# Optimization experiments

Measured on AMD Instinct MI355X. Metric: run time of the kernel, lower is better.

Reference implementation:

```python
import jax, jax.numpy as jnp
import numpy as np

T, B = 4096, 512


def setup_inputs() -> dict:
    key = jax.random.key(0)
    k = jax.random.split(key, 8)
    f32 = jnp.float32
    labels = jax.random.normal(k[0], (T, B, 1), dtype=f32) * 2.0
    logits = jax.random.uniform(k[1], (T, B, 12), dtype=f32)  # normalized params in [0,1]
    uMotor1 = 300.0 + 200.0 * jax.random.uniform(k[2], (T, B, 1), dtype=f32)
    uMotor2 = 300.0 + 200.0 * jax.random.uniform(k[3], (T, B, 1), dtype=f32)
    uMotor3 = 300.0 + 200.0 * jax.random.uniform(k[4], (T, B, 1), dtype=f32)
    uMotor4 = 300.0 + 200.0 * jax.random.uniform(k[5], (T, B, 1), dtype=f32)
    minMotor = 50.0 + 25.0 * jax.random.uniform(k[6], (T, B, 1), dtype=f32)
    maxMotor = 900.0 + 50.0 * jax.random.uniform(k[7], (T, B, 1), dtype=f32)
    return dict(labels=labels, logits=logits, uMotor1=uMotor1, uMotor2=uMotor2,
                uMotor3=uMotor3, uMotor4=uMotor4, maxMotor=maxMotor, minMotor=minMotor)


def _simulate_loss(labels, logits, uMotor1, uMotor2, uMotor3, uMotor4, maxMotor, minMotor):
    mB, g, tau, IRzz, uP = 1.2, 9.81, 0.005, 1e-4, 1.0
    maxChange, max_inc, eps = 95.0, 400.0, 1e-12
    Tn, Bn, _ = logits.shape
    dt = logits.dtype

    gp = lambda kk: logits[:, :, kk]                      # [T, B]
    scale = lambda kk, base: (1.0 + (0.5 - gp(kk)) * maxChange / 100.0) * base
    dxm = scale(0, 0.16); dym = scale(1, 0.16)
    IBxx = scale(3, 0.0123); IByy = scale(4, 0.0123); IBzz = scale(5, 0.0123)
    Cd = scale(6, 0.1)
    kTh = scale(7, 1.076e-5); kTo = scale(8, 1.632e-7)
    tau2 = scale(9, 0.015); kp = scale(10, 1.0); damp = scale(11, 1.0)

    actual_z = labels[:, :, 0]
    u1 = uMotor1[:, :, 0]; u2 = uMotor2[:, :, 0]
    u3 = uMotor3[:, :, 0]; u4 = uMotor4[:, :, 0]
    mn = minMotor[:, :, 0]; mx = maxMotor[:, :, 0]

    hover = jnp.sqrt(jnp.clip(mB * g / (4.0 * kTh.mean() + eps), 1e-6))
    z = jnp.zeros((Bn,), dt)
    one = jnp.ones((Bn,), dt)
    hv = hover * one
    carry0 = (z, z, z,            # x, y, z position
              one, z, z, z,       # quaternion
              z, z, z,            # xdot, ydot, zdot
              z, z, z,            # p, q, r
              hv, hv, hv, hv,     # motor speeds
              z, z, z, z)         # motor accelerations

    xs = (u1[1:], u2[1:], u3[1:], u4[1:], mn[1:], mx[1:],
          damp[1:], tau2[1:], kp[1:], kTh[1:], kTo[1:], Cd[1:],
          IBxx[1:], IByy[1:], IBzz[1:], dxm[1:], dym[1:])

    def step(carry, x):
        (xx, xy, xz, q0, q1, q2, q3, xd, yd, zd, pv, qv, rv,
         w1, w2, w3, w4, wd1, wd2, wd3, wd4) = carry
        (u1c, u2c, u3c, u4c, mnc, mxc, dampc, tau2c, kpc, kThc, kToc, Cdc,
         IBxxc, IByyc, IBzzc, dxmc, dymc) = x
        # 2nd-order motor dynamics (uses un-clamped speeds)
        wdd1 = -2.0 * dampc * tau2c * wd1 - w1 + kpc * u1c / tau2c ** 2
        wdd2 = -2.0 * dampc * tau2c * wd2 - w2 + kpc * u2c / tau2c ** 2
        wdd3 = -2.0 * dampc * tau2c * wd3 - w3 + kpc * u3c / tau2c ** 2
        wdd4 = -2.0 * dampc * tau2c * wd4 - w4 + kpc * u4c / tau2c ** 2
        w1c = jnp.clip(w1, mnc, mxc); w2c = jnp.clip(w2, mnc, mxc)
        w3c = jnp.clip(w3, mnc, mxc); w4c = jnp.clip(w4, mnc, mxc)
        T1 = kThc * w1c ** 2; T2 = kThc * w2c ** 2
        T3 = kThc * w3c ** 2; T4 = kThc * w4c ** 2
        Q1 = kToc * w1c ** 2; Q2 = kToc * w2c ** 2
        Q3 = kToc * w3c ** 2; Q4 = kToc * w4c ** 2
        Thr = T1 + T2 + T3 + T4
        nxd = xd + tau * (Cdc * jnp.sign(-xd) * xd ** 2 + 2.0 * (q0 * q2 + q1 * q3) * Thr) / mB
        nyd = yd + tau * (Cdc * jnp.sign(-yd) * yd ** 2 - 2.0 * (q0 * q1 - q2 * q3) * Thr) / mB
        nzd = zd + tau * (-Cdc * jnp.sign(zd) * zd ** 2 + Thr * (q0 ** 2 - q1 ** 2 - q2 ** 2 + q3 ** 2) - g * mB) / mB
        nq0 = q0 + tau * (-0.5 * pv * q1 - 0.5 * qv * q2 - 0.5 * rv * q3)
        nq1 = q1 + tau * (0.5 * pv * q0 - 0.5 * qv * q3 + 0.5 * rv * q2)
        nq2 = q2 + tau * (0.5 * pv * q3 + 0.5 * qv * q0 - 0.5 * rv * q1)
        nq3 = q3 + tau * (-0.5 * pv * q2 + 0.5 * qv * q1 + 0.5 * rv * q0)
        wsum = w1c - w2c + w3c - w4c
        npv = pv + tau * ((IByyc - IBzzc) * qv * rv - uP * IRzz * wsum * qv + (T1 - T2 - T3 + T4) * dymc) / IBxxc
        nqv = qv + tau * ((IBzzc - IBxxc) * pv * rv + uP * IRzz * wsum * pv + (T1 + T2 - T3 - T4) * dxmc) / IByyc
        nrv = rv + tau * ((IBxxc - IByyc) * pv * qv - Q1 + Q2 - Q3 + Q4) / IBzzc
        nxx = xx + tau * nxd
        nxy = xy + tau * nyd
        nxz_raw = xz + tau * nzd
        nw1 = w1c + tau * wd1; nw2 = w2c + tau * wd2
        nw3 = w3c + tau * wd3; nw4 = w4c + tau * wd4
        nwd1 = wd1 + tau * wdd1; nwd2 = wd2 + tau * wdd2
        nwd3 = wd3 + tau * wdd3; nwd4 = wd4 + tau * wdd4
        mask = jnp.isfinite(nxz_raw) & (jnp.abs(nxz_raw - xz) <= max_inc)
        nxz = jnp.where(mask, nxz_raw, xz)
        new_carry = (nxx, nxy, nxz, nq0, nq1, nq2, nq3, nxd, nyd, nzd,
                     npv, nqv, nrv, nw1, nw2, nw3, nw4, nwd1, nwd2, nwd3, nwd4)
        return new_carry, nxz

    _, z_traj = jax.lax.scan(step, carry0, xs)           # [T-1, B]
    pred_z = jnp.concatenate([jnp.zeros((1, Bn), dt), z_traj], axis=0)  # [T, B]
    return jnp.mean((pred_z - actual_z) ** 2)


def reference(labels, logits, uMotor1, uMotor2, uMotor3, uMotor4, maxMotor, minMotor):
    return _simulate_loss(labels, logits, uMotor1, uMotor2, uMotor3, uMotor4, maxMotor, minMotor)
```

## Files before the change

### kernel.cpp

```cpp
#include <hip/hip_runtime.h>
#include <math.h>

#define T_STEPS 4096
#define B_N     512
#define CHUNK   6
#define NCHF    682

typedef float f2 __attribute__((ext_vector_type(2)));

__device__ __forceinline__ f2 pk_fma(f2 a, f2 b, f2 c){ f2 d; asm("v_pk_fma_f32 %0, %1, %2, %3" : "=v"(d) : "v"(a), "v"(b), "v"(c)); return d; }
__device__ __forceinline__ f2 pk_mul(f2 a, f2 b){ f2 d; asm("v_pk_mul_f32 %0, %1, %2" : "=v"(d) : "v"(a), "v"(b)); return d; }
__device__ __forceinline__ f2 pk_add(f2 a, f2 b){ f2 d; asm("v_pk_add_f32 %0, %1, %2" : "=v"(d) : "v"(a), "v"(b)); return d; }
__device__ __forceinline__ f2 pk_sub(f2 a, f2 b){ f2 d; asm("v_pk_add_f32 %0, %1, %2 neg_lo:[0,1] neg_hi:[0,1]" : "=v"(d) : "v"(a), "v"(b)); return d; }
__device__ __forceinline__ f2 pk_dd(f2 dP){ f2 d; asm("v_pk_add_f32 %0, %1, %1 op_sel:[0,1] op_sel_hi:[0,1] neg_lo:[0,1] neg_hi:[0,0]" : "=v"(d) : "v"(dP)); return d; }
__device__ __forceinline__ f2 pk_vq(f2 a, f2 b){ f2 d; asm("v_pk_add_f32 %0, %1, %2 op_sel:[0,1] op_sel_hi:[1,0]" : "=v"(d) : "v"(a), "v"(b)); return d; }
__device__ __forceinline__ f2 pk_t01a(f2 pq, f2 qA){ f2 d; asm("v_pk_mul_f32 %0, %1, %2 op_sel:[0,1] op_sel_hi:[0,0]" : "=v"(d) : "v"(pq), "v"(qA)); return d; }
__device__ __forceinline__ f2 pk_t01b(f2 pq, f2 qB, f2 acc){ asm("v_pk_fma_f32 %0, %1, %2, %0 op_sel:[1,0,0] op_sel_hi:[1,1,1] neg_hi:[0,1,0]" : "+v"(acc) : "v"(pq), "v"(qB)); return acc; }
__device__ __forceinline__ f2 pk_t01c(f2 rz, f2 qB, f2 acc){ asm("v_pk_fma_f32 %0, %1, %2, %0 op_sel:[0,1,0] op_sel_hi:[0,0,1]" : "+v"(acc) : "v"(rz), "v"(qB)); return acc; }
__device__ __forceinline__ f2 pk_t23a(f2 pq, f2 qA){ f2 d; asm("v_pk_mul_f32 %0, %1, %2 op_sel:[1,0] op_sel_hi:[1,1]" : "=v"(d) : "v"(pq), "v"(qA)); return d; }
__device__ __forceinline__ f2 pk_t23b(f2 pq, f2 qB, f2 acc){ asm("v_pk_fma_f32 %0, %1, %2, %0 op_sel:[0,1,0] op_sel_hi:[0,0,1] neg_hi:[0,1,0]" : "+v"(acc) : "v"(pq), "v"(qB)); return acc; }
__device__ __forceinline__ f2 pk_t23c(f2 rz, f2 qA, f2 acc){ asm("v_pk_fma_f32 %0, %1, %2, %0 op_sel:[0,1,0] op_sel_hi:[0,0,1] neg_lo:[0,1,0]" : "+v"(acc) : "v"(rz), "v"(qA)); return acc; }
__device__ __forceinline__ f2 pk_s1p(f2 pq, f2 rz){ f2 d; asm("v_pk_mul_f32 %0, %1, %2 op_sel:[1,0] op_sel_hi:[0,0]" : "=v"(d) : "v"(pq), "v"(rz)); return d; }
__device__ __forceinline__ f2 pk_s2p(f2 pq, f2 ws){ f2 d; asm("v_pk_mul_f32 %0, %1, %2 op_sel:[1,0] op_sel_hi:[0,1]" : "=v"(d) : "v"(pq), "v"(ws)); return d; }

union PkU { float4 v[5]; };

struct CarryP {
  f2 w12, w34, wd12, wd34, qA, qB, pq, rz;
  float xz;
};

__device__ __forceinline__ void stepP(CarryP& c, const float4* F, float& facc,
                                      f2 TT, f2 HT, f2 HP) {
  const float TAU = 0.005f, TAUG = 0.04905f;
  f2 KU12 = {F[0].x, F[0].y}, KU34 = {F[0].z, F[0].w};
  f2 AA   = {F[1].x, F[1].y};
  float mn = F[1].z, mx = F[1].w;
  f2 cAC = {F[2].x, F[2].y}, cBD = {F[2].z, F[2].w};
  f2 cdymxm = {F[3].x, F[3].y};
  float cE = F[3].z, cq = F[3].w;
  float cthr = F[4].x, mcdx = F[4].y, label = F[4].z;

  f2 wdd12 = pk_sub(pk_fma(AA, c.wd12, KU12), c.w12);
  f2 wdd34 = pk_sub(pk_fma(AA, c.wd34, KU34), c.w34);
  f2 wc12, wc34;
  wc12.x = fminf(fmaxf(c.w12.x, mn), mx); wc12.y = fminf(fmaxf(c.w12.y, mn), mx);
  wc34.x = fminf(fmaxf(c.w34.x, mn), mx); wc34.y = fminf(fmaxf(c.w34.y, mn), mx);
  f2 s12 = pk_mul(wc12, wc12), s34 = pk_mul(wc34, wc34);
  f2 aP = pk_add(s12, s34);
  f2 dP = pk_sub(s12, s34);
  float ssum = aP.x + aP.y;
  float dqd  = aP.y - aP.x;
  f2 dd = pk_dd(dP);
  f2 tw = pk_add(wc12, wc34);
  float wsum = tw.x - tw.y;
  f2 qs1 = pk_mul(c.qA, c.qA), qs2 = pk_mul(c.qB, c.qB);
  f2 vq = pk_vq(qs1, qs2);
  float qq = vq.x - vq.y;
  float zd = c.rz.y;
  float zdm = zd * fabsf(zd);
  float nzd = fmaf(mcdx, zdm, zd);
  float Thr2 = cthr * ssum;
  nzd = fmaf(Thr2, qq, nzd) - TAUG;
  f2 t01 = pk_t01a(c.pq, c.qA);
  t01 = pk_t01b(c.pq, c.qB, t01);
  t01 = pk_t01c(c.rz, c.qB, t01);
  f2 t23 = pk_t23a(c.pq, c.qA);
  t23 = pk_t23b(c.pq, c.qB, t23);
  t23 = pk_t23c(c.rz, c.qA, t23);
  f2 nqA = pk_fma(HT, t01, c.qA);
  f2 nqB = pk_fma(HP, t23, c.qB);
  f2 sp1 = pk_s1p(c.pq, c.rz);
  f2 ws2 = {wsum, wsum};
  f2 sp2 = pk_s2p(c.pq, ws2);
  f2 npq = pk_fma(cAC, sp1, c.pq);
  npq = pk_fma(cBD, sp2, npq);
  npq = pk_fma(cdymxm, dd, npq);
  float nrv = fmaf(cE, c.pq.x * c.pq.y, c.rz.x);
  nrv = fmaf(cq, dqd, nrv);
  float nxz = fmaf(TAU, nzd, c.xz);
  float dlt = nxz - c.xz;
  float xznew = (fabsf(dlt) <= 400.0f) ? nxz : c.xz;
  float e = xznew - label;
  facc = fmaf(e, e, facc);
  f2 nw12 = pk_fma(TT, c.wd12, wc12);
  f2 nw34 = pk_fma(TT, c.wd34, wc34);
  c.wd12 = pk_fma(TT, wdd12, c.wd12);
  c.wd34 = pk_fma(TT, wdd34, c.wd34);
  c.w12 = nw12; c.w34 = nw34;
  c.qA = nqA; c.qB = nqB; c.pq = npq;
  c.rz = f2{nrv, nzd}; c.xz = xznew;
}

struct Pk {
  float KU1, KU2, KU3, KU4, A, mn, mx, cthr;
  float cdym, cdxm, cq, cdx, cA, cB, cC, cD, cE, label, pad0, pad1;
};
__device__ __forceinline__ float sc_ref(float g, float base) {
  return (1.0f + (0.5f - g) * 0.95f) * base;
}
struct Carry {
  float xz, q0, q1, q2, q3, zd, pv, qv, rv;
  float w1, w2, w3, w4, wd1, wd2, wd3, wd4;
};
__device__ __forceinline__ Pk computePk(size_t i,
    const float* __restrict__ logits,
    const float* __restrict__ u1, const float* __restrict__ u2,
    const float* __restrict__ u3, const float* __restrict__ u4,
    const float* __restrict__ mxM, const float* __restrict__ mnM,
    const float* __restrict__ labels) {
  const float4* lg = (const float4*)logits + i * 3;
  float4 l0 = lg[0], l1 = lg[1], l2 = lg[2];
  float dxm  = sc_ref(l0.x, 0.16f);
  float dym  = sc_ref(l0.y, 0.16f);
  float IBxx = sc_ref(l0.w, 0.0123f);
  float IByy = sc_ref(l1.x, 0.0123f);
  float IBzz = sc_ref(l1.y, 0.0123f);
  float Cd   = sc_ref(l1.z, 0.1f);
  float kTh  = sc_ref(l1.w, 1.076e-05f);
  float kTo  = sc_ref(l2.x, 1.632e-07f);
  float tau2 = sc_ref(l2.y, 0.015f);
  float kp   = sc_ref(l2.z, 1.0f);
  float damp = sc_ref(l2.w, 1.0f);
  const float tau = 0.005f, tauOverMb = tau / 1.2f;
  Pk p;
  float K = kp / (tau2 * tau2);
  p.KU1 = K * u1[i];  p.KU2 = K * u2[i];  p.KU3 = K * u3[i];  p.KU4 = K * u4[i];
  p.A = -2.0f * damp * tau2;
  p.mn = mnM[i];  p.mx = mxM[i];
  p.cthr = kTh * tauOverMb;
  float tx = tau / IBxx, ty = tau / IByy, tz = tau / IBzz;
  p.cdym = kTh * dym * tx;  p.cdxm = kTh * dxm * ty;
  p.cq = kTo * tz;  p.cdx = Cd * tauOverMb;
  p.cA = (IByy - IBzz) * tx;  p.cB = 1e-04f * tx;
  p.cC = (IBzz - IBxx) * ty;  p.cD = 1e-04f * ty;
  p.cE = (IBxx - IByy) * tz;
  p.label = labels[i];  p.pad0 = 0.f; p.pad1 = 0.f;
  return p;
}
__device__ __forceinline__ void stepOne(Carry& c, const Pk& p, float& facc) {
  const float TAU = 0.005f, HTAU = 0.0025f, TAUG = 0.04905f;
  float wdd1 = fmaf(p.A, c.wd1, p.KU1) - c.w1;
  float wdd2 = fmaf(p.A, c.wd2, p.KU2) - c.w2;
  float wdd3 = fmaf(p.A, c.wd3, p.KU3) - c.w3;
  float wdd4 = fmaf(p.A, c.wd4, p.KU4) - c.w4;
  float w1c = fminf(fmaxf(c.w1, p.mn), p.mx);
  float w2c = fminf(fmaxf(c.w2, p.mn), p.mx);
  float w3c = fminf(fmaxf(c.w3, p.mn), p.mx);
  float w4c = fminf(fmaxf(c.w4, p.mn), p.mx);
  float s1 = w1c*w1c, s2 = w2c*w2c, s3 = w3c*w3c, s4 = w4c*w4c;
  float sA = s1+s3, sB = s2+s4, ssum = sA+sB;
  float dymd = (s1+s4)-(s2+s3), dxmd = (s1+s2)-(s3+s4), dqd = sB-sA;
  float Thr2 = p.cthr * ssum;
  float qq = fmaf(c.q0,c.q0,c.q3*c.q3) - fmaf(c.q1,c.q1,c.q2*c.q2);
  float zdm = c.zd * fabsf(c.zd);
  float nzd = fmaf(-p.cdx, zdm, c.zd);
  nzd = fmaf(Thr2, qq, nzd) - TAUG;
  float t0 = fmaf(c.pv,c.q1, fmaf(c.qv,c.q2,  c.rv*c.q3));
  float t1 = fmaf(c.pv,c.q0, fmaf(-c.qv,c.q3, c.rv*c.q2));
  float t2 = fmaf(c.pv,c.q3, fmaf(c.qv,c.q0, -(c.rv*c.q1)));
  float t3 = fmaf(-c.pv,c.q2, fmaf(c.qv,c.q1, c.rv*c.q0));
  float nq0 = fmaf(-HTAU,t0,c.q0), nq1 = fmaf(HTAU,t1,c.q1);
  float nq2 = fmaf(HTAU,t2,c.q2),  nq3 = fmaf(HTAU,t3,c.q3);
  float wsum = (w1c-w2c)+(w3c-w4c);
  float npv = fmaf(p.cA, c.qv*c.rv, c.pv);
  npv = fmaf(-p.cB, wsum*c.qv, npv); npv = fmaf(p.cdym, dymd, npv);
  float nqv = fmaf(p.cC, c.pv*c.rv, c.qv);
  nqv = fmaf(p.cD, wsum*c.pv, nqv);  nqv = fmaf(p.cdxm, dxmd, nqv);
  float nrv = fmaf(p.cE, c.pv*c.qv, c.rv);
  nrv = fmaf(p.cq, dqd, nrv);
  float nxz = fmaf(TAU, nzd, c.xz);
  float d = nxz - c.xz;
  float xznew = (fabsf(d) <= 400.0f) ? nxz : c.xz;
  float e = xznew - p.label;
  facc = fmaf(e, e, facc);
  c.w1 = fmaf(TAU,c.wd1,w1c); c.w2 = fmaf(TAU,c.wd2,w2c);
  c.w3 = fmaf(TAU,c.wd3,w3c); c.w4 = fmaf(TAU,c.wd4,w4c);
  c.wd1 = fmaf(TAU,wdd1,c.wd1); c.wd2 = fmaf(TAU,wdd2,c.wd2);
  c.wd3 = fmaf(TAU,wdd3,c.wd3); c.wd4 = fmaf(TAU,wdd4,c.wd4);
  c.q0=nq0; c.q1=nq1; c.q2=nq2; c.q3=nq3;
  c.pv=npv; c.qv=nqv; c.rv=nrv; c.zd=nzd; c.xz=xznew;
}

__device__ __forceinline__ void gload_lds16(const void* g, void* l) {
  __builtin_amdgcn_global_load_lds(
      (const __attribute__((address_space(1))) void*)g,
      (__attribute__((address_space(3))) void*)l, 16, 0, 0);
}

__global__ void k_kth(const float* __restrict__ logits, float* __restrict__ partial) {
  __shared__ float sm[256];
  float a = 0.f;
  const int n = T_STEPS * B_N;
  for (int i = blockIdx.x * 256 + threadIdx.x; i < n; i += 1024 * 256)
    a += (1.0f + (0.5f - logits[(size_t)i * 12 + 7]) * 0.95f) * 1.076e-05f;
  sm[threadIdx.x] = a; __syncthreads();
  for (int s = 128; s; s >>= 1) {
    if (threadIdx.x < s) sm[threadIdx.x] += sm[threadIdx.x + s];
    __syncthreads();
  }
  if (threadIdx.x == 0) partial[blockIdx.x] = sm[0];
}

__global__ void k_hover(const float* __restrict__ partial, float* __restrict__ hover) {
  __shared__ float sm[1024];
  sm[threadIdx.x] = partial[threadIdx.x];
  __syncthreads();
  for (int s = 512; s; s >>= 1) {
    if (threadIdx.x < s) sm[threadIdx.x] += sm[threadIdx.x + s];
    __syncthreads();
  }
  if (threadIdx.x == 0) {
    float mean = sm[0] * (1.0f / 2097152.0f);
    float h = 1.2f * 9.81f / (4.0f * mean + 1e-12f);
    hover[0] = sqrtf(fmaxf(h, 1e-06f));
  }
}

__global__ void k_pre(const float* __restrict__ logits,
                      const float* __restrict__ u1, const float* __restrict__ u2,
                      const float* __restrict__ u3, const float* __restrict__ u4,
                      const float* __restrict__ mxM, const float* __restrict__ mnM,
                      const float* __restrict__ labels, float4* __restrict__ pack) {
  size_t i = (size_t)blockIdx.x * 256 + threadIdx.x;
  const float4* lg = (const float4*)logits + i * 3;
  float4 l0 = lg[0], l1 = lg[1], l2 = lg[2];
  float dxm  = sc_ref(l0.x, 0.16f);
  float dym  = sc_ref(l0.y, 0.16f);
  float IBxx = sc_ref(l0.w, 0.0123f);
  float IByy = sc_ref(l1.x, 0.0123f);
  float IBzz = sc_ref(l1.y, 0.0123f);
  float Cd   = sc_ref(l1.z, 0.1f);
  float kTh  = sc_ref(l1.w, 1.076e-05f);
  float kTo  = sc_ref(l2.x, 1.632e-07f);
  float tau2 = sc_ref(l2.y, 0.015f);
  float kp   = sc_ref(l2.z, 1.0f);
  float damp = sc_ref(l2.w, 1.0f);
  const float tau = 0.005f, tauOverMb = tau / 1.2f;
  float K = kp / (tau2 * tau2);
  float A = -2.0f * damp * tau2;
  float tx = tau / IBxx, ty = tau / IByy, tz = tau / IBzz;
  float4* dst = pack + i * 5;
  dst[0] = float4{K * u1[i], K * u2[i], K * u3[i], K * u4[i]};
  dst[1] = float4{A, A, mnM[i], mxM[i]};
  dst[2] = float4{(IByy - IBzz) * tx, (IBzz - IBxx) * ty, -1e-04f * tx, 1e-04f * ty};
  dst[3] = float4{kTh * dym * tx, kTh * dxm * ty, (IBxx - IByy) * tz, kTo * tz};
  dst[4] = float4{kTh * tauOverMb, -(Cd * tauOverMb), labels[i], 0.f};
}

__global__ __launch_bounds__(128, 1) void k_simpc(
    const float4* __restrict__ pack,
    const float* __restrict__ labels,
    const float* __restrict__ hoverp, double* __restrict__ bsum) {
  __shared__ float4 lds[4][CHUNK][5][64];
  const int lane = threadIdx.x & 63;
  const int wid  = threadIdx.x >> 6;
  const int b = blockIdx.x * 64 + lane;

  const char* packb = (const char*)pack + (size_t)b * 80;

  auto stage = [&](int chS, int bufS) {
    float4* dstb = &lds[bufS][0][0][0];
    #pragma unroll
    for (int s = 0; s < CHUNK; ++s) {
      int t = 1 + chS * CHUNK + s;
      if (t > T_STEPS - 1) t = T_STEPS - 1;
      const char* src = packb + (size_t)t * (B_N * 80);
      #pragma unroll
      for (int k = 0; k < 5; ++k)
        gload_lds16(src + 16 * k, (void*)(dstb + (s * 5 + k) * 64));
    }
  };

  if (wid == 1) {
    stage(0, 0);
    stage(1, 1);
    asm volatile("s_waitcnt vmcnt(30)" ::: "memory");
  }
  __syncthreads();

  CarryP c;
  double acc = 0.0;
  f2 TT = {0.005f, 0.005f}, HT = {-0.0025f, 0.0025f}, HP = {0.0025f, 0.0025f};
  if (wid == 0) {
    float hv = hoverp[0];
    c.w12 = f2{hv, hv}; c.w34 = f2{hv, hv};
    c.wd12 = f2{0.f, 0.f}; c.wd34 = f2{0.f, 0.f};
    c.qA = f2{1.f, 0.f}; c.qB = f2{0.f, 0.f};
    c.pq = f2{0.f, 0.f}; c.rz = f2{0.f, 0.f}; c.xz = 0.f;
    float l0 = labels[b];
    acc = (double)l0 * (double)l0;
  }

  PkU pA, pB;
  for (int ch = 0; ch < NCHF; ++ch) {
    if (wid == 1) {
      int chS = ch + 2; if (chS > NCHF) chS = NCHF;
      stage(chS, (ch + 2) & 3);
      asm volatile("s_waitcnt vmcnt(30)" ::: "memory");
    }
    __syncthreads();
    if (wid == 0) {
      const float4* Lb = &lds[ch & 3][0][0][0];
      float facc = 0.f;
      #pragma unroll
      for (int k = 0; k < 5; ++k) pA.v[k] = Lb[k * 64 + lane];
      #pragma unroll
      for (int s = 0; s < CHUNK; ++s) {
        PkU& cur = (s & 1) ? pB : pA;
        PkU& nxt = (s & 1) ? pA : pB;
        if (s + 1 < CHUNK) {
          #pragma unroll
          for (int k = 0; k < 5; ++k) nxt.v[k] = Lb[((s + 1) * 5 + k) * 64 + lane];
        }
        stepP(c, cur.v, facc, TT, HT, HP);
      }
      acc += (double)facc;
    }
  }
  if (wid == 0) {
    const float4* Lb = &lds[NCHF & 3][0][0][0];
    float facc = 0.f;
    #pragma unroll
    for (int k = 0; k < 5; ++k) pA.v[k] = Lb[k * 64 + lane];
    #pragma unroll
    for (int s = 0; s < 3; ++s) {
      PkU& cur = (s & 1) ? pB : pA;
      PkU& nxt = (s & 1) ? pA : pB;
      if (s + 1 < 3) {
        #pragma unroll
        for (int k = 0; k < 5; ++k) nxt.v[k] = Lb[((s + 1) * 5 + k) * 64 + lane];
      }
      stepP(c, cur.v, facc, TT, HT, HP);
    }
    acc += (double)facc;
    bsum[b] = acc;
  } else {
    asm volatile("s_waitcnt vmcnt(0)" ::: "memory");
  }
}

__global__ __launch_bounds__(64, 1) void k_sim_fb(
    const float* __restrict__ logits,
    const float* __restrict__ u1, const float* __restrict__ u2,
    const float* __restrict__ u3, const float* __restrict__ u4,
    const float* __restrict__ mxM, const float* __restrict__ mnM,
    const float* __restrict__ labels,
    const float* __restrict__ hoverp, double* __restrict__ bsum) {
  int b = blockIdx.x * 64 + threadIdx.x;
  float hv = hoverp[0];
  Carry c;
  c.xz = 0.f; c.q0 = 1.f; c.q1 = 0.f; c.q2 = 0.f; c.q3 = 0.f;
  c.zd = 0.f; c.pv = 0.f; c.qv = 0.f; c.rv = 0.f;
  c.w1 = hv; c.w2 = hv; c.w3 = hv; c.w4 = hv;
  c.wd1 = 0.f; c.wd2 = 0.f; c.wd3 = 0.f; c.wd4 = 0.f;
  float l0 = labels[b];
  double acc = (double)l0 * (double)l0;
  for (int t = 1; t < T_STEPS; ++t) {
    Pk p = computePk((size_t)t * B_N + b, logits, u1, u2, u3, u4, mxM, mnM, labels);
    float facc = 0.f;
    stepOne(c, p, facc);
    acc += (double)facc;
  }
  bsum[b] = acc;
}

__global__ void k_final(const double* __restrict__ bsum, float* __restrict__ out) {
  __shared__ double sm[512];
  sm[threadIdx.x] = bsum[threadIdx.x];
  __syncthreads();
  for (int s = 256; s; s >>= 1) {
    if (threadIdx.x < s) sm[threadIdx.x] += sm[threadIdx.x + s];
    __syncthreads();
  }
  if (threadIdx.x == 0) out[0] = (float)(sm[0] * (1.0 / 2097152.0));
}

extern "C" void kernel_launch(void* const* d_in, const int* in_sizes, int n_in,
                              void* d_out, int out_size, void* d_ws, size_t ws_size,
                              hipStream_t stream) {
  const float* labels = (const float*)d_in[0];
  const float* logits = (const float*)d_in[1];
  const float* u1 = (const float*)d_in[2];
  const float* u2 = (const float*)d_in[3];
  const float* u3 = (const float*)d_in[4];
  const float* u4 = (const float*)d_in[5];
  const float* mxM = (const float*)d_in[6];
  const float* mnM = (const float*)d_in[7];
  float* out = (float*)d_out;

  char* ws = (char*)d_ws;
  float*  hover   = (float*)(ws);
  float*  partial = (float*)(ws + 256);
  double* bsum    = (double*)(ws + 8192);
  float4* pack    = (float4*)(ws + 16384);
  size_t need = 16384 + (size_t)T_STEPS * B_N * 80;
  bool pre = (ws_size >= need);

  k_kth  <<<1024, 256, 0, stream>>>(logits, partial);
  k_hover<<<1, 1024, 0, stream>>>(partial, hover);
  if (pre) {
    k_pre<<<8192, 256, 0, stream>>>(logits, u1, u2, u3, u4, mxM, mnM, labels, pack);
    k_simpc<<<8, 128, 0, stream>>>(pack, labels, hover, bsum);
  } else {
    k_sim_fb<<<8, 64, 0, stream>>>(logits, u1, u2, u3, u4, mxM, mnM, labels, hover, bsum);
  }
  k_final<<<1, 512, 0, stream>>>(bsum, out);
}
```

Before: 719.7 us.

## Split motor dynamics into producer wave, pipeline through LDS to body-dynamics wave

The sequential scan is split across two wavefronts. The loader wave now also integrates the motor-speed recurrence one chunk ahead and writes the derived squared-speed sums, differences and wsum to LDS. The second wave consumes these to integrate attitude, position and loss, which shortens the critical serial dependency chain per step. Buffers rotate three ways with one barrier per chunk, and clamping uses med3. The cost is extra LDS traffic and added synchronisation coupling between the two waves.

After: 928.2 us. +29.0%, slower.

```diff
diff --git a/kernel.cpp b/kernel.cpp
--- a/kernel.cpp
+++ b/kernel.cpp
@@ -13,6 +13,7 @@
 __device__ __forceinline__ f2 pk_add(f2 a, f2 b){ f2 d; asm("v_pk_add_f32 %0, %1, %2" : "=v"(d) : "v"(a), "v"(b)); return d; }
 __device__ __forceinline__ f2 pk_sub(f2 a, f2 b){ f2 d; asm("v_pk_add_f32 %0, %1, %2 neg_lo:[0,1] neg_hi:[0,1]" : "=v"(d) : "v"(a), "v"(b)); return d; }
 __device__ __forceinline__ f2 pk_dd(f2 dP){ f2 d; asm("v_pk_add_f32 %0, %1, %1 op_sel:[0,1] op_sel_hi:[0,1] neg_lo:[0,1] neg_hi:[0,0]" : "=v"(d) : "v"(dP)); return d; }
+__device__ __forceinline__ f2 pk_dq(f2 aP){ f2 d; asm("v_pk_add_f32 %0, %1, %1 op_sel:[0,1] op_sel_hi:[0,1] neg_lo:[1,0] neg_hi:[0,0]" : "=v"(d) : "v"(aP)); return d; }
 __device__ __forceinline__ f2 pk_vq(f2 a, f2 b){ f2 d; asm("v_pk_add_f32 %0, %1, %2 op_sel:[0,1] op_sel_hi:[1,0]" : "=v"(d) : "v"(a), "v"(b)); return d; }
 __device__ __forceinline__ f2 pk_t01a(f2 pq, f2 qA){ f2 d; asm("v_pk_mul_f32 %0, %1, %2 op_sel:[0,1] op_sel_hi:[0,0]" : "=v"(d) : "v"(pq), "v"(qA)); return d; }
 __device__ __forceinline__ f2 pk_t01b(f2 pq, f2 qB, f2 acc){ asm("v_pk_fma_f32 %0, %1, %2, %0 op_sel:[1,0,0] op_sel_hi:[1,1,1] neg_hi:[0,1,0]" : "+v"(acc) : "v"(pq), "v"(qB)); return acc; }
@@ -22,75 +23,8 @@
 __device__ __forceinline__ f2 pk_t23c(f2 rz, f2 qA, f2 acc){ asm("v_pk_fma_f32 %0, %1, %2, %0 op_sel:[0,1,0] op_sel_hi:[0,0,1] neg_lo:[0,1,0]" : "+v"(acc) : "v"(rz), "v"(qA)); return acc; }
 __device__ __forceinline__ f2 pk_s1p(f2 pq, f2 rz){ f2 d; asm("v_pk_mul_f32 %0, %1, %2 op_sel:[1,0] op_sel_hi:[0,0]" : "=v"(d) : "v"(pq), "v"(rz)); return d; }
 __device__ __forceinline__ f2 pk_s2p(f2 pq, f2 ws){ f2 d; asm("v_pk_mul_f32 %0, %1, %2 op_sel:[1,0] op_sel_hi:[0,1]" : "=v"(d) : "v"(pq), "v"(ws)); return d; }
-
-union PkU { float4 v[5]; };
-
-struct CarryP {
-  f2 w12, w34, wd12, wd34, qA, qB, pq, rz;
-  float xz;
-};
-
-__device__ __forceinline__ void stepP(CarryP& c, const float4* F, float& facc,
-                                      f2 TT, f2 HT, f2 HP) {
-  const float TAU = 0.005f, TAUG = 0.04905f;
-  f2 KU12 = {F[0].x, F[0].y}, KU34 = {F[0].z, F[0].w};
-  f2 AA   = {F[1].x, F[1].y};
-  float mn = F[1].z, mx = F[1].w;
-  f2 cAC = {F[2].x, F[2].y}, cBD = {F[2].z, F[2].w};
-  f2 cdymxm = {F[3].x, F[3].y};
-  float cE = F[3].z, cq = F[3].w;
-  float cthr = F[4].x, mcdx = F[4].y, label = F[4].z;
-
-  f2 wdd12 = pk_sub(pk_fma(AA, c.wd12, KU12), c.w12);
-  f2 wdd34 = pk_sub(pk_fma(AA, c.wd34, KU34), c.w34);
-  f2 wc12, wc34;
-  wc12.x = fminf(fmaxf(c.w12.x, mn), mx); wc12.y = fminf(fmaxf(c.w12.y, mn), mx);
-  wc34.x = fminf(fmaxf(c.w34.x, mn), mx); wc34.y = fminf(fmaxf(c.w34.y, mn), mx);
-  f2 s12 = pk_mul(wc12, wc12), s34 = pk_mul(wc34, wc34);
-  f2 aP = pk_add(s12, s34);
-  f2 dP = pk_sub(s12, s34);
-  float ssum = aP.x + aP.y;
-  float dqd  = aP.y - aP.x;
-  f2 dd = pk_dd(dP);
-  f2 tw = pk_add(wc12, wc34);
-  float wsum = tw.x - tw.y;
-  f2 qs1 = pk_mul(c.qA, c.qA), qs2 = pk_mul(c.qB, c.qB);
-  f2 vq = pk_vq(qs1, qs2);
-  float qq = vq.x - vq.y;
-  float zd = c.rz.y;
-  float zdm = zd * fabsf(zd);
-  float nzd = fmaf(mcdx, zdm, zd);
-  float Thr2 = cthr * ssum;
-  nzd = fmaf(Thr2, qq, nzd) - TAUG;
-  f2 t01 = pk_t01a(c.pq, c.qA);
-  t01 = pk_t01b(c.pq, c.qB, t01);
-  t01 = pk_t01c(c.rz, c.qB, t01);
-  f2 t23 = pk_t23a(c.pq, c.qA);
-  t23 = pk_t23b(c.pq, c.qB, t23);
-  t23 = pk_t23c(c.rz, c.qA, t23);
-  f2 nqA = pk_fma(HT, t01, c.qA);
-  f2 nqB = pk_fma(HP, t23, c.qB);
-  f2 sp1 = pk_s1p(c.pq, c.rz);
-  f2 ws2 = {wsum, wsum};
-  f2 sp2 = pk_s2p(c.pq, ws2);
-  f2 npq = pk_fma(cAC, sp1, c.pq);
-  npq = pk_fma(cBD, sp2, npq);
-  npq = pk_fma(cdymxm, dd, npq);
-  float nrv = fmaf(cE, c.pq.x * c.pq.y, c.rz.x);
-  nrv = fmaf(cq, dqd, nrv);
-  float nxz = fmaf(TAU, nzd, c.xz);
-  float dlt = nxz - c.xz;
-  float xznew = (fabsf(dlt) <= 400.0f) ? nxz : c.xz;
-  float e = xznew - label;
-  facc = fmaf(e, e, facc);
-  f2 nw12 = pk_fma(TT, c.wd12, wc12);
-  f2 nw34 = pk_fma(TT, c.wd34, wc34);
-  c.wd12 = pk_fma(TT, wdd12, c.wd12);
-  c.wd34 = pk_fma(TT, wdd34, c.wd34);
-  c.w12 = nw12; c.w34 = nw34;
-  c.qA = nqA; c.qB = nqB; c.pq = npq;
-  c.rz = f2{nrv, nzd}; c.xz = xznew;
-}
+__device__ __forceinline__ float med3f(float x, float a, float b){ float d; asm("v_med3_f32 %0, %1, %2, %3" : "=v"(d) : "v"(x), "v"(a), "v"(b)); return d; }
+
 
 struct Pk {
   float KU1, KU2, KU3, KU4, A, mn, mx, cthr;
@@ -248,19 +182,23 @@
   dst[4] = float4{kTh * tauOverMb, -(Cd * tauOverMb), labels[i], 0.f};
 }
 
-__global__ __launch_bounds__(128, 1) void k_simpc(
+__global__ __launch_bounds__(128, 1) void k_simms(
     const float4* __restrict__ pack,
     const float* __restrict__ labels,
     const float* __restrict__ hoverp, double* __restrict__ bsum) {
-  __shared__ float4 lds[4][CHUNK][5][64];
+  __shared__ float4 pprm[3][CHUNK][5][64];
+  __shared__ float4 outs4[3][CHUNK][64];
+  __shared__ float  outs1[3][CHUNK][64];
   const int lane = threadIdx.x & 63;
   const int wid  = threadIdx.x >> 6;
   const int b = blockIdx.x * 64 + lane;
 
   const char* packb = (const char*)pack + (size_t)b * 80;
+  const f2 TT = {0.005f, 0.005f};
+  const f2 HT = {-0.0025f, 0.0025f};
+  const f2 HP = {0.0025f, 0.0025f};
 
   auto stage = [&](int chS, int bufS) {
-    float4* dstb = &lds[bufS][0][0][0];
     #pragma unroll
     for (int s = 0; s < CHUNK; ++s) {
       int t = 1 + chS * CHUNK + s;
@@ -268,70 +206,154 @@
       const char* src = packb + (size_t)t * (B_N * 80);
       #pragma unroll
       for (int k = 0; k < 5; ++k)
-        gload_lds16(src + 16 * k, (void*)(dstb + (s * 5 + k) * 64));
+        gload_lds16(src + 16 * k, (void*)&pprm[bufS][s][k][0]);
     }
   };
 
+  f2 w12, w34, wd12, wd34;
+  auto motor_chunk = [&](int pb, int ob) {
+    float4 F0 = pprm[pb][0][0][lane];
+    float4 F1 = pprm[pb][0][1][lane];
+    #pragma unroll
+    for (int s = 0; s < CHUNK; ++s) {
+      float4 nF0, nF1;
+      if (s + 1 < CHUNK) { nF0 = pprm[pb][s+1][0][lane]; nF1 = pprm[pb][s+1][1][lane]; }
+      f2 KU12 = {F0.x, F0.y}, KU34 = {F0.z, F0.w};
+      f2 AA   = {F1.x, F1.y};
+      float mn = F1.z, mx = F1.w;
+      f2 wdd12 = pk_sub(pk_fma(AA, wd12, KU12), w12);
+      f2 wdd34 = pk_sub(pk_fma(AA, wd34, KU34), w34);
+      f2 wc12, wc34;
+      wc12.x = med3f(w12.x, mn, mx); wc12.y = med3f(w12.y, mn, mx);
+      wc34.x = med3f(w34.x, mn, mx); wc34.y = med3f(w34.y, mn, mx);
+      f2 s12 = pk_mul(wc12, wc12), s34 = pk_mul(wc34, wc34);
+      f2 aP = pk_add(s12, s34);
+      f2 dP = pk_sub(s12, s34);
+      f2 dq = pk_dq(aP);
+      f2 dd = pk_dd(dP);
+      f2 tw = pk_add(wc12, wc34);
+      float wsum = tw.x - tw.y;
+      outs4[ob][s][lane] = float4{dq.x, dq.y, dd.x, dd.y};
+      outs1[ob][s][lane] = wsum;
+      f2 nw12 = pk_fma(TT, wd12, wc12);
+      f2 nw34 = pk_fma(TT, wd34, wc34);
+      wd12 = pk_fma(TT, wdd12, wd12);
+      wd34 = pk_fma(TT, wdd34, wd34);
+      w12 = nw12; w34 = nw34;
+      F0 = nF0; F1 = nF1;
+    }
+  };
+
+  f2 qA, qB, pq, rz;
+  float xz;
+  double acc = 0.0;
+
+  auto stepB = [&](float4 F2, float4 F3, float4 F4, float4 G, float ws, float& facc) {
+    const float TAU = 0.005f, TAUG = 0.04905f;
+    f2 cAC = {F2.x, F2.y}, cBD = {F2.z, F2.w};
+    f2 cdymxm = {F3.x, F3.y};
+    float cE = F3.z, cq = F3.w;
+    float cthr = F4.x, mcdx = F4.y, label = F4.z;
+    f2 dqv = {G.x, G.y};
+    f2 dd  = {G.z, G.w};
+    f2 qs1 = pk_mul(qA, qA), qs2 = pk_mul(qB, qB);
+    f2 vq = pk_vq(qs1, qs2);
+    float qq = vq.x - vq.y;
+    float zd = rz.y;
+    float zdm = zd * fabsf(zd);
+    float nzd = fmaf(mcdx, zdm, zd);
+    float Thr2 = cthr * dqv.y;
+    nzd = fmaf(Thr2, qq, nzd) - TAUG;
+    f2 t01 = pk_t01a(pq, qA);
+    t01 = pk_t01b(pq, qB, t01);
+    t01 = pk_t01c(rz, qB, t01);
+    f2 t23 = pk_t23a(pq, qA);
+    t23 = pk_t23b(pq, qB, t23);
+    t23 = pk_t23c(rz, qA, t23);
+    f2 nqA = pk_fma(HT, t01, qA);
+    f2 nqB = pk_fma(HP, t23, qB);
+    f2 sp1 = pk_s1p(pq, rz);
+    f2 ws2 = {ws, ws};
+    f2 sp2 = pk_s2p(pq, ws2);
+    f2 npq = pk_fma(cAC, sp1, pq);
+    npq = pk_fma(cBD, sp2, npq);
+    npq = pk_fma(cdymxm, dd, npq);
+    float nrv = fmaf(cE, pq.x * pq.y, rz.x);
+    nrv = fmaf(cq, dqv.x, nrv);
+    float nxz = fmaf(TAU, nzd, xz);
+    float dlt = nxz - xz;
+    float xznew = (fabsf(dlt) <= 400.0f) ? nxz : xz;
+    float e = xznew - label;
+    facc = fmaf(e, e, facc);
+    qA = nqA; qB = nqB; pq = npq;
+    rz = f2{nrv, nzd}; xz = xznew;
+  };
+
+  struct SetB { float4 F2, F3, F4, G; float ws; };
+  auto loadB = [&](SetB& S, int pb, int s) {
+    S.F2 = pprm[pb][s][2][lane];
+    S.F3 = pprm[pb][s][3][lane];
+    S.F4 = pprm[pb][s][4][lane];
+    S.G  = outs4[pb][s][lane];
+    S.ws = outs1[pb][s][lane];
+  };
+
   if (wid == 1) {
-    stage(0, 0);
-    stage(1, 1);
+    float hv = hoverp[0];
+    w12 = f2{hv, hv}; w34 = f2{hv, hv};
+    wd12 = f2{0.f, 0.f}; wd34 = f2{0.f, 0.f};
+    stage(0, 0); stage(1, 1);
     asm volatile("s_waitcnt vmcnt(30)" ::: "memory");
-  }
-  __syncthreads();
-
-  CarryP c;
-  double acc = 0.0;
-  f2 TT = {0.005f, 0.005f}, HT = {-0.0025f, 0.0025f}, HP = {0.0025f, 0.0025f};
-  if (wid == 0) {
-    float hv = hoverp[0];
-    c.w12 = f2{hv, hv}; c.w34 = f2{hv, hv};
-    c.wd12 = f2{0.f, 0.f}; c.wd34 = f2{0.f, 0.f};
-    c.qA = f2{1.f, 0.f}; c.qB = f2{0.f, 0.f};
-    c.pq = f2{0.f, 0.f}; c.rz = f2{0.f, 0.f}; c.xz = 0.f;
+    __builtin_amdgcn_sched_barrier(0);
+    motor_chunk(0, 0);
+    asm volatile("s_waitcnt lgkmcnt(0)" ::: "memory");
+    __builtin_amdgcn_sched_barrier(0);
+  } else {
+    float hv = hoverp[0]; (void)hv;
+    qA = f2{1.f, 0.f}; qB = f2{0.f, 0.f};
+    pq = f2{0.f, 0.f}; rz = f2{0.f, 0.f}; xz = 0.f;
     float l0 = labels[b];
     acc = (double)l0 * (double)l0;
   }
-
-  PkU pA, pB;
-  for (int ch = 0; ch < NCHF; ++ch) {
+  __syncthreads();
+
+  int pw = 2, pa = 1, pbuf = 0;
+  for (int i = 0; i < NCHF; ++i) {
     if (wid == 1) {
-      int chS = ch + 2; if (chS > NCHF) chS = NCHF;
-      stage(chS, (ch + 2) & 3);
+      int chS = i + 2; if (chS > NCHF) chS = NCHF;
+      stage(chS, pw);
       asm volatile("s_waitcnt vmcnt(30)" ::: "memory");
-    }
-    __syncthreads();
-    if (wid == 0) {
-      const float4* Lb = &lds[ch & 3][0][0][0];
+      __builtin_amdgcn_sched_barrier(0);
+      motor_chunk(pa, pa);
+      asm volatile("s_waitcnt lgkmcnt(0)" ::: "memory");
+      __builtin_amdgcn_sched_barrier(0);
+    } else {
+      SetB sa, sb;
       float facc = 0.f;
-      #pragma unroll
-      for (int k = 0; k < 5; ++k) pA.v[k] = Lb[k * 64 + lane];
+      loadB(sa, pbuf, 0);
       #pragma unroll
       for (int s = 0; s < CHUNK; ++s) {
-        PkU& cur = (s & 1) ? pB : pA;
-        PkU& nxt = (s & 1) ? pA : pB;
-        if (s + 1 < CHUNK) {
-          #pragma unroll
-          for (int k = 0; k < 5; ++k) nxt.v[k] = Lb[((s + 1) * 5 + k) * 64 + lane];
-        }
-        stepP(c, cur.v, facc, TT, HT, HP);
+        SetB& cur = (s & 1) ? sb : sa;
+        SetB& nxt = (s & 1) ? sa : sb;
+        if (s + 1 < CHUNK) loadB(nxt, pbuf, s + 1);
+        stepB(cur.F2, cur.F3, cur.F4, cur.G, cur.ws, facc);
       }
       acc += (double)facc;
     }
-  }
+    __syncthreads();
+    int t = pw; pw = pbuf; pbuf = pa; pa = t;
+  }
+
   if (wid == 0) {
-    const float4* Lb = &lds[NCHF & 3][0][0][0];
+    SetB sa, sb;
     float facc = 0.f;
-    #pragma unroll
-    for (int k = 0; k < 5; ++k) pA.v[k] = Lb[k * 64 + lane];
+    loadB(sa, pbuf, 0);
     #pragma unroll
     for (int s = 0; s < 3; ++s) {
-      PkU& cur = (s & 1) ? pB : pA;
-      PkU& nxt = (s & 1) ? pA : pB;
-      if (s + 1 < 3) {
-        #pragma unroll
-        for (int k = 0; k < 5; ++k) nxt.v[k] = Lb[((s + 1) * 5 + k) * 64 + lane];
-      }
-      stepP(c, cur.v, facc, TT, HT, HP);
+      SetB& cur = (s & 1) ? sb : sa;
+      SetB& nxt = (s & 1) ? sa : sb;
+      if (s + 1 < 3) loadB(nxt, pbuf, s + 1);
+      stepB(cur.F2, cur.F3, cur.F4, cur.G, cur.ws, facc);
     }
     acc += (double)facc;
     bsum[b] = acc;
@@ -401,7 +423,7 @@
   k_hover<<<1, 1024, 0, stream>>>(partial, hover);
   if (pre) {
     k_pre<<<8192, 256, 0, stream>>>(logits, u1, u2, u3, u4, mxM, mnM, labels, pack);
-    k_simpc<<<8, 128, 0, stream>>>(pack, labels, hover, bsum);
+    k_simms<<<8, 128, 0, stream>>>(pack, labels, hover, bsum);
   } else {
     k_sim_fb<<<8, 64, 0, stream>>>(logits, u1, u2, u3, u4, mxM, mnM, labels, hover, bsum);
   }
```
